# Kernel optimization log

Measured on AMD Instinct MI355X. Metric: run time of the kernel, lower is better.

## Reference

```python
import jax, jax.numpy as jnp
import numpy as np

NEG_INF = -1e30  # stand-in for float('-inf'); avoids inf-inf NaN edge cases, same softmax result


def setup_inputs() -> dict:
    key = jax.random.key(0)
    k1, k2, k3, k4, k5 = jax.random.split(key, 5)
    B, T, C, H = 16, 2048, 200, 64
    x = jax.random.normal(k1, (B, T, C), dtype=jnp.float32)
    # padding mask over key positions, broadcastable to [B, T, T]
    padding_mask = jax.random.randint(k2, (B, 1, T), 0, 2, dtype=jnp.int32)
    # nn.Linear(n_embd, head_size, bias=False) weights, stored as [C, H] so y = x @ W
    Wk = jax.random.normal(k3, (C, H), dtype=jnp.float32) * (C ** -0.5)
    Wq = jax.random.normal(k4, (C, H), dtype=jnp.float32) * (C ** -0.5)
    Wv = jax.random.normal(k5, (C, H), dtype=jnp.float32) * (C ** -0.5)
    return {"x": x, "padding_mask": padding_mask, "Wk": Wk, "Wq": Wq, "Wv": Wv}


def reference(x, padding_mask, Wk, Wq, Wv):
    # x: [B,T,C]; padding_mask: [B,1,T] (0 = padded key position)
    k = x @ Wk  # [B,T,H]
    q = x @ Wq  # [B,T,H]
    v = x @ Wv  # [B,T,H]
    scale = k.shape[-1] ** -0.5
    wei = jnp.einsum("bqh,bkh->bqk", q, k) * scale  # [B,T,T]
    # mask padded key columns before softmax
    wei = jnp.where(padding_mask == 0, NEG_INF, wei)
    wei = jax.nn.softmax(wei, axis=-1)
    # mask padded query rows (transpose of padding mask) to exact zero after softmax
    mask_t = jnp.swapaxes(padding_mask, -2, -1)  # [B,T,1]
    wei = jnp.where(mask_t == 0, 0.0, wei)
    # dropout is identity in eval mode
    out = jnp.einsum("bqk,bkh->bqh", wei, v)  # [B,T,H]
    return out
```

## Files before the change

### kernel.cpp

```cpp
#include <hip/hip_runtime.h>


typedef __attribute__((ext_vector_type(8))) __bf16 bf16x8;
typedef __attribute__((ext_vector_type(4))) __bf16 bf16x4;
typedef __attribute__((ext_vector_type(4))) float f32x4;

#define T_SEQ 2048
#define C_DIM 200
#define H_DIM 64
#define BT_TOT 32768
#define QKV_ELEMS 2097152
#define PROW 136
#define OPAD 68
#define WTF_FULL 36864
#define WTF_ELEMS 38400
#define WTF_A_ELEMS 24576
#define LOG2E 1.44269504088896f

__global__ void prep_w(const float* __restrict__ Wk, const float* __restrict__ Wq,
                       const float* __restrict__ Wv, __bf16* __restrict__ WtF) {
    int idx = blockIdx.x * 256 + threadIdx.x;
    if (idx >= WTF_ELEMS) return;
    int w, c, h;
    if (idx < WTF_FULL) {
        int j = idx & 7, lane = (idx >> 3) & 63;
        int chunk = idx >> 9;
        int t = chunk & 3, rest = chunk >> 2;
        w = rest % 3; int ks = rest / 3;
        c = ks * 32 + (lane >> 4) * 8 + j;
        h = t * 16 + (lane & 15);
    } else {
        int i2 = idx - WTF_FULL;
        int j = i2 & 7, l15 = (i2 >> 3) & 15, t = (i2 >> 7) & 3;
        w = i2 >> 9;
        c = 192 + j;
        h = t * 16 + l15;
    }
    const float* W = (w == 0) ? Wq : (w == 1) ? Wk : Wv;
    float val = W[c * H_DIM + h];
    if (w == 0) val *= 0.125f * LOG2E;
    WtF[idx] = (__bf16)val;
}

__global__ __launch_bounds__(256) void qkv_proj(const float* __restrict__ x,
                                                const __bf16* __restrict__ WtF,
                                                __bf16* __restrict__ qb,
                                                __bf16* __restrict__ kb,
                                                __bf16* __restrict__ vT) {
    __shared__ __bf16 Wl[WTF_A_ELEMS];

    const int tid = threadIdx.x;
    const int wave = tid >> 6, lane = tid & 63, l15 = lane & 15, quad = lane >> 4;
    const int m0b = blockIdx.x * 64;
    const int row0 = m0b + wave * 16;

    f32x4 acc[3][4] = {};

    #pragma unroll
    for (int i = 0; i < 12; ++i) {
        const int c = i * 256 + tid;
        *(bf16x8*)(Wl + c * 8) = *(const bf16x8*)(WtF + c * 8);
    }
    __syncthreads();
    #pragma unroll
    for (int ks = 0; ks < 4; ++ks) {
        const float* xr = x + (size_t)(row0 + l15) * C_DIM + ks * 32 + quad * 8;
        const float4 f0 = *(const float4*)xr;
        const float4 f1 = *(const float4*)(xr + 4);
        bf16x8 a;
        a[0]=(__bf16)f0.x; a[1]=(__bf16)f0.y; a[2]=(__bf16)f0.z; a[3]=(__bf16)f0.w;
        a[4]=(__bf16)f1.x; a[5]=(__bf16)f1.y; a[6]=(__bf16)f1.z; a[7]=(__bf16)f1.w;
        #pragma unroll
        for (int w = 0; w < 3; ++w)
            #pragma unroll
            for (int t = 0; t < 4; ++t) {
                const bf16x8 bf = *(const bf16x8*)(Wl + ((ks * 12 + w * 4 + t) << 9) + lane * 8);
                acc[w][t] = __builtin_amdgcn_mfma_f32_16x16x32_bf16(a, bf, acc[w][t], 0, 0, 0);
            }
    }
    __syncthreads();

    #pragma unroll
    for (int i = 0; i < 7; ++i) {
        const int c = i * 256 + tid;
        if (c < 1728)
            *(bf16x8*)(Wl + c * 8) = *(const bf16x8*)(WtF + WTF_A_ELEMS + c * 8);
    }
    __syncthreads();
    #pragma unroll
    for (int ks = 4; ks < 7; ++ks) {
        bf16x8 a;
        if (ks < 6 || quad == 0) {
            const float* xr = x + (size_t)(row0 + l15) * C_DIM + ks * 32 + quad * 8;
            const float4 f0 = *(const float4*)xr;
            const float4 f1 = *(const float4*)(xr + 4);
            a[0]=(__bf16)f0.x; a[1]=(__bf16)f0.y; a[2]=(__bf16)f0.z; a[3]=(__bf16)f0.w;
            a[4]=(__bf16)f1.x; a[5]=(__bf16)f1.y; a[6]=(__bf16)f1.z; a[7]=(__bf16)f1.w;
        } else {
            #pragma unroll
            for (int j = 0; j < 8; ++j) a[j] = (__bf16)0.f;
        }
        #pragma unroll
        for (int w = 0; w < 3; ++w)
            #pragma unroll
            for (int t = 0; t < 4; ++t) {
                const int off = (ks < 6) ? (((ks - 4) * 12 + w * 4 + t) << 9) + lane * 8
                                         : 12288 + ((w * 4 + t) << 7) + l15 * 8;
                const bf16x8 bf = *(const bf16x8*)(Wl + off);
                acc[w][t] = __builtin_amdgcn_mfma_f32_16x16x32_bf16(a, bf, acc[w][t], 0, 0, 0);
            }
    }

    #pragma unroll
    for (int t = 0; t < 4; ++t)
        #pragma unroll
        for (int r = 0; r < 4; ++r) {
            const size_t m = row0 + quad * 4 + r;
            qb[m * H_DIM + t * 16 + l15] = (__bf16)acc[0][t][r];
            kb[m * H_DIM + t * 16 + l15] = (__bf16)acc[1][t][r];
        }
    __syncthreads();
    #pragma unroll
    for (int t = 0; t < 4; ++t)
        #pragma unroll
        for (int r = 0; r < 4; ++r)
            Wl[(t * 16 + l15) * 72 + wave * 16 + quad * 4 + r] = (__bf16)acc[2][t][r];
    __syncthreads();
    const int bb = m0b >> 11, tloc = m0b & 2047;
    #pragma unroll
    for (int i = 0; i < 2; ++i) {
        const int seg = i * 256 + tid;
        const int h = seg >> 3, s8 = seg & 7;
        *(bf16x8*)(vT + ((size_t)bb * H_DIM + h) * T_SEQ + tloc + s8 * 8) =
            *(const bf16x8*)(Wl + h * 72 + s8 * 8);
    }
}

__global__ __launch_bounds__(256, 2) void attn(const __bf16* __restrict__ qb,
                                               const __bf16* __restrict__ kb,
                                               const __bf16* __restrict__ vT,
                                               const int* __restrict__ pm,
                                               float* __restrict__ out) {
    __shared__ __align__(16) char arena[8192 + 69632 + 1024];
    float* biasS = (float*)arena;

    const int tid = threadIdx.x;
    const int wave = tid >> 6, lane = tid & 63, l15 = lane & 15, quad = lane >> 4;
    const int ks = wave;
    const int b = blockIdx.y;
    const int q0 = blockIdx.x * 64;
    const size_t bT = (size_t)b * T_SEQ;

    for (int i = tid; i < 512; i += 256) {
        const int4 p4 = *(const int4*)(pm + bT + i * 4);
        biasS[i * 4 + 0] = p4.x ? 0.f : -1e30f;
        biasS[i * 4 + 1] = p4.y ? 0.f : -1e30f;
        biasS[i * 4 + 2] = p4.z ? 0.f : -1e30f;
        biasS[i * 4 + 3] = p4.w ? 0.f : -1e30f;
    }
    __syncthreads();

    bf16x8 qa[4][2];
    #pragma unroll
    for (int mt = 0; mt < 4; ++mt)
        #pragma unroll
        for (int s = 0; s < 2; ++s)
            qa[mt][s] = *(const bf16x8*)(qb + (bT + q0 + mt * 16 + l15) * H_DIM + s * 32 + quad * 8);

    __bf16* P = (__bf16*)(arena + 8192) + wave * (64 * PROW);
    const __bf16* kbase = kb + bT * H_DIM;
    const __bf16* vbase = vT + (size_t)b * H_DIM * T_SEQ;

    f32x4 oacc[4][4] = {};
    float lsum[4] = {};

    for (int kt = 0; kt < 4; ++kt) {
        const int key0 = ks * 512 + kt * 128;

        #pragma unroll
        for (int n = 0; n < 8; ++n) {
            const f32x4 bias = *(const f32x4*)(biasS + key0 + n * 16 + quad * 4);
            bf16x8 kf[2];
            #pragma unroll
            for (int s = 0; s < 2; ++s)
                kf[s] = *(const bf16x8*)(kbase + (key0 + n * 16 + l15) * H_DIM + s * 32 + quad * 8);
            f32x4 s_[4];
            #pragma unroll
            for (int mt = 0; mt < 4; ++mt) s_[mt] = bias;
            #pragma unroll
            for (int s = 0; s < 2; ++s)
                #pragma unroll
                for (int mt = 0; mt < 4; ++mt)
                    s_[mt] = __builtin_amdgcn_mfma_f32_16x16x32_bf16(kf[s], qa[mt][s], s_[mt], 0, 0, 0);
            #pragma unroll
            for (int mt = 0; mt < 4; ++mt) {
                bf16x4 p4;
                #pragma unroll
                for (int r = 0; r < 4; ++r) {
                    const float e = exp2f(s_[mt][r]);
                    lsum[mt] += e;
                    p4[r] = (__bf16)e;
                }
                *(bf16x4*)(P + (mt * 16 + l15) * PROW + n * 16 + quad * 4) = p4;
            }
        }

        bf16x8 pa[4][4];
        #pragma unroll
        for (int mt = 0; mt < 4; ++mt)
            #pragma unroll
            for (int s = 0; s < 4; ++s)
                pa[mt][s] = *(const bf16x8*)(P + (mt * 16 + l15) * PROW + s * 32 + quad * 8);

        #pragma unroll
        for (int t = 0; t < 4; ++t) {
            bf16x8 vf[4];
            #pragma unroll
            for (int s = 0; s < 4; ++s)
                vf[s] = *(const bf16x8*)(vbase + (size_t)(t * 16 + l15) * T_SEQ + key0 + s * 32 + quad * 8);
            #pragma unroll
            for (int s = 0; s < 4; ++s)
                #pragma unroll
                for (int mt = 0; mt < 4; ++mt)
                    oacc[mt][t] = __builtin_amdgcn_mfma_f32_16x16x32_bf16(pa[mt][s], vf[s], oacc[mt][t], 0, 0, 0);
        }
    }

    #pragma unroll
    for (int mt = 0; mt < 4; ++mt) {
        lsum[mt] += __shfl_xor(lsum[mt], 16, 64);
        lsum[mt] += __shfl_xor(lsum[mt], 32, 64);
    }

    float* Ocomb = (float*)(arena + 8192);
    float* Lcomb = (float*)(arena + 8192 + 69632);

    __syncthreads();
    {
        float* Ow = Ocomb + wave * (64 * OPAD);
        #pragma unroll
        for (int mt = 0; mt < 4; ++mt) {
            #pragma unroll
            for (int t = 0; t < 4; ++t)
                #pragma unroll
                for (int r = 0; r < 4; ++r)
                    Ow[(mt * 16 + quad * 4 + r) * OPAD + t * 16 + l15] = oacc[mt][t][r];
            if (quad == 0) Lcomb[wave * 64 + mt * 16 + l15] = lsum[mt];
        }
    }
    __syncthreads();
    {
        const int mt = wave;
        #pragma unroll
        for (int r = 0; r < 4; ++r) {
            const int rw = mt * 16 + quad * 4 + r;
            const int qpos = q0 + rw;
            float lv = 0.f;
            #pragma unroll
            for (int wv = 0; wv < 4; ++wv) lv += Lcomb[wv * 64 + rw];
            const bool qvalid = biasS[qpos] == 0.f;
            const float inv = (qvalid && lv > 0.f) ? 1.f / lv : 0.f;
            #pragma unroll
            for (int t = 0; t < 4; ++t) {
                float o = 0.f;
                #pragma unroll
                for (int wv = 0; wv < 4; ++wv)
                    o += Ocomb[wv * (64 * OPAD) + rw * OPAD + t * 16 + l15];
                out[(bT + qpos) * H_DIM + t * 16 + l15] = o * inv;
            }
        }
    }
}

extern "C" void kernel_launch(void* const* d_in, const int* in_sizes, int n_in,
                              void* d_out, int out_size, void* d_ws, size_t ws_size,
                              hipStream_t stream) {
    const float* x  = (const float*)d_in[0];
    const int* pm   = (const int*)d_in[1];
    const float* Wk = (const float*)d_in[2];
    const float* Wq = (const float*)d_in[3];
    const float* Wv = (const float*)d_in[4];
    float* out = (float*)d_out;

    __bf16* qb  = (__bf16*)d_ws;
    __bf16* kb  = qb + QKV_ELEMS;
    __bf16* vT  = kb + QKV_ELEMS;
    __bf16* WtF = vT + QKV_ELEMS;

    prep_w<<<dim3((WTF_ELEMS + 255) / 256), dim3(256), 0, stream>>>(Wk, Wq, Wv, WtF);
    qkv_proj<<<dim3(BT_TOT / 64), dim3(256), 0, stream>>>(x, WtF, qb, kb, vT);
    attn<<<dim3(T_SEQ / 64, 16), dim3(256), 0, stream>>>(qb, kb, vT, pm, out);
}
```

Before: 125.5 us.

## Compute softmax row sums via MFMA with ones vector and stage QKV stores through LDS

The attention kernel stops accumulating the softmax denominator with scalar adds and cross-lane shuffles. Instead it runs an extra MFMA of the bf16 probability tile against a ones vector, so the sum is taken over the rounded values actually used in P·V. The projection kernel now stages Q, K and V tiles in shared memory and writes all three with coalesced 16-byte stores, replacing the scattered 2-byte global stores for Q and K. The cost is 16 extra MFMAs per key tile, another accumulator register set, and more LDS traffic in the projection epilogue.

```diff
diff --git a/kernel.cpp b/kernel.cpp
--- a/kernel.cpp
+++ b/kernel.cpp
@@ -111,28 +111,35 @@
             }
     }
 
-    #pragma unroll
-    for (int t = 0; t < 4; ++t)
-        #pragma unroll
-        for (int r = 0; r < 4; ++r) {
-            const size_t m = row0 + quad * 4 + r;
-            qb[m * H_DIM + t * 16 + l15] = (__bf16)acc[0][t][r];
-            kb[m * H_DIM + t * 16 + l15] = (__bf16)acc[1][t][r];
-        }
-    __syncthreads();
-    #pragma unroll
-    for (int t = 0; t < 4; ++t)
-        #pragma unroll
-        for (int r = 0; r < 4; ++r)
-            Wl[(t * 16 + l15) * 72 + wave * 16 + quad * 4 + r] = (__bf16)acc[2][t][r];
-    __syncthreads();
-    const int bb = m0b >> 11, tloc = m0b & 2047;
-    #pragma unroll
-    for (int i = 0; i < 2; ++i) {
-        const int seg = i * 256 + tid;
-        const int h = seg >> 3, s8 = seg & 7;
-        *(bf16x8*)(vT + ((size_t)bb * H_DIM + h) * T_SEQ + tloc + s8 * 8) =
-            *(const bf16x8*)(Wl + h * 72 + s8 * 8);
+    __syncthreads();
+    {
+        __bf16* Lq = Wl;
+        __bf16* Lk = Wl + 4608;
+        __bf16* Lv = Wl + 9216;
+        #pragma unroll
+        for (int t = 0; t < 4; ++t)
+            #pragma unroll
+            for (int r = 0; r < 4; ++r) {
+                const int mloc = wave * 16 + quad * 4 + r;
+                Lq[mloc * 72 + t * 16 + l15] = (__bf16)acc[0][t][r];
+                Lk[mloc * 72 + t * 16 + l15] = (__bf16)acc[1][t][r];
+                Lv[(t * 16 + l15) * 72 + mloc] = (__bf16)acc[2][t][r];
+            }
+    }
+    __syncthreads();
+    {
+        const int bb = m0b >> 11, tloc = m0b & 2047;
+        #pragma unroll
+        for (int i = 0; i < 2; ++i) {
+            const int seg = i * 256 + tid;
+            const int row = seg >> 3, s8 = seg & 7;
+            *(bf16x8*)(qb + (size_t)(m0b + row) * H_DIM + s8 * 8) =
+                *(const bf16x8*)(Wl + row * 72 + s8 * 8);
+            *(bf16x8*)(kb + (size_t)(m0b + row) * H_DIM + s8 * 8) =
+                *(const bf16x8*)(Wl + 4608 + row * 72 + s8 * 8);
+            *(bf16x8*)(vT + ((size_t)bb * H_DIM + row) * T_SEQ + tloc + s8 * 8) =
+                *(const bf16x8*)(Wl + 9216 + row * 72 + s8 * 8);
+        }
     }
 }
 
@@ -167,12 +174,16 @@
         for (int s = 0; s < 2; ++s)
             qa[mt][s] = *(const bf16x8*)(qb + (bT + q0 + mt * 16 + l15) * H_DIM + s * 32 + quad * 8);
 
+    bf16x8 ones;
+    #pragma unroll
+    for (int j = 0; j < 8; ++j) ones[j] = (__bf16)1.0f;
+
     __bf16* P = (__bf16*)(arena + 8192) + wave * (64 * PROW);
     const __bf16* kbase = kb + bT * H_DIM;
     const __bf16* vbase = vT + (size_t)b * H_DIM * T_SEQ;
 
     f32x4 oacc[4][4] = {};
-    float lsum[4] = {};
+    f32x4 oaccL[4] = {};
 
     for (int kt = 0; kt < 4; ++kt) {
         const int key0 = ks * 512 + kt * 128;
@@ -196,11 +207,8 @@
             for (int mt = 0; mt < 4; ++mt) {
                 bf16x4 p4;
                 #pragma unroll
-                for (int r = 0; r < 4; ++r) {
-                    const float e = exp2f(s_[mt][r]);
-                    lsum[mt] += e;
-                    p4[r] = (__bf16)e;
-                }
+                for (int r = 0; r < 4; ++r)
+                    p4[r] = (__bf16)exp2f(s_[mt][r]);
                 *(bf16x4*)(P + (mt * 16 + l15) * PROW + n * 16 + quad * 4) = p4;
             }
         }
@@ -213,6 +221,12 @@
                 pa[mt][s] = *(const bf16x8*)(P + (mt * 16 + l15) * PROW + s * 32 + quad * 8);
 
         #pragma unroll
+        for (int s = 0; s < 4; ++s)
+            #pragma unroll
+            for (int mt = 0; mt < 4; ++mt)
+                oaccL[mt] = __builtin_amdgcn_mfma_f32_16x16x32_bf16(pa[mt][s], ones, oaccL[mt], 0, 0, 0);
+
+        #pragma unroll
         for (int t = 0; t < 4; ++t) {
             bf16x8 vf[4];
             #pragma unroll
@@ -226,12 +240,6 @@
         }
     }
 
-    #pragma unroll
-    for (int mt = 0; mt < 4; ++mt) {
-        lsum[mt] += __shfl_xor(lsum[mt], 16, 64);
-        lsum[mt] += __shfl_xor(lsum[mt], 32, 64);
-    }
-
     float* Ocomb = (float*)(arena + 8192);
     float* Lcomb = (float*)(arena + 8192 + 69632);
 
@@ -245,7 +253,11 @@
                 #pragma unroll
                 for (int r = 0; r < 4; ++r)
                     Ow[(mt * 16 + quad * 4 + r) * OPAD + t * 16 + l15] = oacc[mt][t][r];
-            if (quad == 0) Lcomb[wave * 64 + mt * 16 + l15] = lsum[mt];
+            if (l15 == 0) {
+                #pragma unroll
+                for (int r = 0; r < 4; ++r)
+                    Lcomb[wave * 64 + mt * 16 + quad * 4 + r] = oaccL[mt][r];
+            }
         }
     }
     __syncthreads();
```

Result: no change. 125.2 us (-0.2%).
